# Optimization experiments

Hardware: AMD Instinct MI355X
Metric: run time of the kernel (lower is better)

Reference implementation:

```python
import jax, jax.numpy as jnp
import numpy as np

B, IN_DIM, C, H, W = 4, 64, 128, 64, 64
HW = H * W
EPS = 1e-5


def _conv(x, w, b, pad):
    y = jax.lax.conv_general_dilated(
        x, w, (1, 1), [(pad, pad), (pad, pad)],
        dimension_numbers=('NCHW', 'OIHW', 'NCHW'))
    return y + b[None, :, None, None]


def _ln_chw(x, g, b):
    # torch LayerNorm([C,H,W]): normalize over (C,H,W) per sample, affine per-element
    m = jnp.mean(x, axis=(1, 2, 3), keepdims=True)
    v = jnp.mean((x - m) ** 2, axis=(1, 2, 3), keepdims=True)
    return (x - m) * jax.lax.rsqrt(v + EPS) * g[None] + b[None]


def _lrelu(x):
    return jnp.where(x >= 0, x, 0.01 * x)


def setup_inputs():
    ks = jax.random.split(jax.random.key(0), 16)

    def n(i, shape, s):
        return jax.random.normal(ks[i], shape, jnp.float32) * s

    inp = {
        'f_e': n(0, (B, IN_DIM, H, W), 1.0),
        'f_i': n(1, (B, IN_DIM, H, W), 1.0),
        'w1': n(2, (C, IN_DIM, 3, 3), 0.04), 'b1': jnp.zeros((C,), jnp.float32),
        'g1': jnp.ones((C, H, W), jnp.float32), 'be1': jnp.zeros((C, H, W), jnp.float32),
        'w2': n(3, (C, IN_DIM, 3, 3), 0.04), 'b2': jnp.zeros((C,), jnp.float32),
        'g2': jnp.ones((C, H, W), jnp.float32), 'be2': jnp.zeros((C, H, W), jnp.float32),
        'W3': n(4, (HW, HW), 0.015), 'b3': jnp.zeros((HW,), jnp.float32),
        'W4': n(5, (C, C), 0.08), 'b4': jnp.zeros((C,), jnp.float32),
        'W5': n(6, (C, C), 0.08), 'b5': jnp.zeros((C,), jnp.float32),
        'w6a': n(7, (C, C, 1, 1), 0.08), 'b6a': jnp.zeros((C,), jnp.float32),
        'g6a': jnp.ones((C, H, W), jnp.float32), 'be6a': jnp.zeros((C, H, W), jnp.float32),
        'w6b': n(8, (C, C, 3, 3), 0.03), 'b6b': jnp.zeros((C,), jnp.float32),
        'g6b': jnp.ones((C, H, W), jnp.float32), 'be6b': jnp.zeros((C, H, W), jnp.float32),
        'wf': n(9, (IN_DIM, C, 1, 1), 0.08), 'bf': jnp.zeros((IN_DIM,), jnp.float32),
    }
    return inp


def reference(f_e, f_i, w1, b1, g1, be1, w2, b2, g2, be2, W3, b3, W4, b4,
              W5, b5, w6a, b6a, g6a, be6a, w6b, b6b, g6b, be6b, wf, bf):
    b_, _, h, w = f_e.shape
    c = w1.shape[0]
    hw = h * w

    # f_1: conv3x3 -> LN([C,H,W]) -> LeakyReLU -> b (hw) c
    x1 = _lrelu(_ln_chw(_conv(f_e, w1, b1, 1), g1, be1))
    f_e_1 = x1.transpose(0, 2, 3, 1).reshape(b_, hw, c)

    # f_2: conv3x3 -> LN -> LeakyReLU (stays b c h w)
    f_i_2 = _lrelu(_ln_chw(_conv(f_i, w2, b2, 1), g2, be2))

    # f_3: b c (hw) -> Linear(HW,HW) -> LeakyReLU
    f_i_3 = _lrelu(jnp.einsum('bcn,mn->bcm', f_i_2.reshape(b_, c, hw), W3) + b3)

    # f_4: b (hw) c -> Linear(C,C) -> LeakyReLU
    tok = f_i_2.transpose(0, 2, 3, 1).reshape(b_, hw, c)
    f_e_4 = _lrelu(jnp.einsum('bnc,dc->bnd', tok, W4) + b4)

    # unscaled single-head attention over hw tokens
    scores = jnp.einsum('bnc,bcm->bnm', f_e_4, f_i_3)   # (b, hw, hw)
    attn = jax.nn.softmax(scores, axis=-1)
    f_e_5_in = jnp.einsum('bnm,bmc->bnc', attn, f_e_1)

    # f_5: Linear(C,C) -> LeakyReLU -> b c h w
    f_e_5 = _lrelu(jnp.einsum('bnc,dc->bnd', f_e_5_in, W5) + b5)
    f_e_5 = f_e_5.reshape(b_, h, w, c).transpose(0, 3, 1, 2)

    # f_6: conv1x1 -> LN -> LReLU -> conv3x3 -> LN -> LReLU
    y = _lrelu(_ln_chw(_conv(f_i_2, w6a, b6a, 0), g6a, be6a))
    f_i_6 = _lrelu(_ln_chw(_conv(y, w6b, b6b, 1), g6b, be6b))

    f_e_7 = f_e_5 * f_i_6
    f_e_8 = _conv(f_e_7, wf, bf, 0)
    return (f_e_8, f_i_2)
```

## Files before the change

kernel.cpp:

```cpp
#include <hip/hip_runtime.h>

typedef unsigned short ushort_t;
typedef unsigned int uint_t;
typedef unsigned long long u64_t;

#define Bn 4
#define IND 64
#define Cn 128
#define Nn 4096
#define CN 524288
#define BUF 2097152

typedef __attribute__((ext_vector_type(8))) __bf16 bf16x8;
typedef __attribute__((ext_vector_type(4))) float f32x4;

__device__ __forceinline__ float b2f(ushort_t s) {
    return __uint_as_float(((uint_t)s) << 16);
}
__device__ __forceinline__ ushort_t f2b(float f) {
    uint_t u = __float_as_uint(f);
    uint_t r = u + 0x7fffu + ((u >> 16) & 1u);
    return (ushort_t)(r >> 16);
}
__device__ __forceinline__ void unpack8(uint4 u, float* f) {
    f[0] = __uint_as_float(u.x << 16); f[1] = __uint_as_float(u.x & 0xffff0000u);
    f[2] = __uint_as_float(u.y << 16); f[3] = __uint_as_float(u.y & 0xffff0000u);
    f[4] = __uint_as_float(u.z << 16); f[5] = __uint_as_float(u.z & 0xffff0000u);
    f[6] = __uint_as_float(u.w << 16); f[7] = __uint_as_float(u.w & 0xffff0000u);
}
__device__ __forceinline__ float lrelu(float x) { return x >= 0.f ? x : 0.01f * x; }

__device__ __forceinline__ float getv(const float* p, size_t i) { return p[i]; }
__device__ __forceinline__ float getv(const ushort_t* p, size_t i) { return b2f(p[i]); }
__device__ __forceinline__ float4 get4(const float* p, size_t i) { return *(const float4*)(p + i); }
__device__ __forceinline__ float4 get4(const ushort_t* p, size_t i) {
    ushort4 u = *(const ushort4*)(p + i);
    float4 f = {b2f(u.x), b2f(u.y), b2f(u.z), b2f(u.w)};
    return f;
}
__device__ __forceinline__ void stv(float* p, float v) { *p = v; }
__device__ __forceinline__ void stv(ushort_t* p, float v) { *p = f2b(v); }

__device__ __forceinline__ uint4 pack8(float4 a, float4 b) {
    uint4 r;
    r.x = (uint_t)f2b(a.x) | ((uint_t)f2b(a.y) << 16);
    r.y = (uint_t)f2b(a.z) | ((uint_t)f2b(a.w) << 16);
    r.z = (uint_t)f2b(b.x) | ((uint_t)f2b(b.y) << 16);
    r.w = (uint_t)f2b(b.z) | ((uint_t)f2b(b.w) << 16);
    return r;
}

__global__ void detect_kernel(const void* g1, int* flag) {
    if (threadIdx.x == 0 && blockIdx.x == 0)
        *flag = (((const ushort_t*)g1)[0] == 0x3F80) ? 0 : 1;
}

template <int CI>
__global__ __launch_bounds__(256) void wtrans(const void* w, ushort_t* Wt, const int* flagp) {
    int F = *flagp;
    int idx = blockIdx.x * 256 + threadIdx.x;
    if (idx >= 128 * 9 * CI) return;
    int co = idx / (9 * CI);
    int rem = idx - co * 9 * CI;
    int tap = rem / CI;
    int ci = rem - tap * CI;
    size_t srci = (size_t)co * CI * 9 + (size_t)ci * 9 + tap;
    float v = F ? ((const float*)w)[srci] : b2f(((const ushort_t*)w)[srci]);
    Wt[idx] = f2b(v);
}

template <typename TEXT>
__device__ __forceinline__ void tin_body(const TEXT* src, ushort_t* dst, float (*tile)[33]) {
    int b = blockIdx.z, c0 = blockIdx.y * 32, n0 = blockIdx.x * 32;
    int nx = threadIdx.x & 31, cy = threadIdx.x >> 5;
    #pragma unroll
    for (int s = 0; s < 4; s++) {
        int cl = cy + s * 8;
        tile[cl][nx] = getv(src, ((size_t)(b * 64 + c0 + cl)) * 4096 + n0 + nx);
    }
    __syncthreads();
    #pragma unroll
    for (int s = 0; s < 4; s++) {
        int nl = cy + s * 8;
        dst[((size_t)b * 4096 + n0 + nl) * 64 + c0 + nx] = f2b(tile[nx][nl]);
    }
}

__global__ __launch_bounds__(256) void transpose_in(const void* src, ushort_t* dst, const int* flagp) {
    __shared__ float tile[32][33];
    int F = *flagp;
    if (F) tin_body((const float*)src, dst, tile);
    else   tin_body((const ushort_t*)src, dst, tile);
}

template <int CI>
__global__ __launch_bounds__(512) void conv_mfma(const ushort_t* __restrict__ Xt,
                                                 const ushort_t* __restrict__ Wt,
                                                 const void* bias, float* __restrict__ out,
                                                 const int* flagp) {
    constexpr int RS = CI + 8;
    constexpr int SROWS = 195;
    constexpr int SBYTES = SROWS * RS * 2;
    constexpr int OBYTES = 128 * 68 * 4;
    constexpr int SMEM = SBYTES > OBYTES ? SBYTES : OBYTES;
    __shared__ __align__(16) char smem[SMEM];
    ushort_t* S = (ushort_t*)smem;
    float* Ob = (float*)smem;

    int t = threadIdx.x;
    int blk = blockIdx.x;
    int b = blk >> 6, y = blk & 63;
    int n0 = y << 6;

    constexpr int RQ = CI / 8;
    constexpr int CNT = SROWS * RQ;
    for (int i = t; i < CNT; i += 512) {
        int s = i / RQ;
        int c8 = (i - s * RQ) * 8;
        int tok = n0 + s - 65;
        uint4 v = {0u, 0u, 0u, 0u};
        if (s < 194 && (unsigned)tok < 4096u)
            v = *(const uint4*)(Xt + ((size_t)b * 4096 + tok) * CI + c8);
        *(uint4*)(S + (size_t)s * RS + c8) = v;
    }
    __syncthreads();

    int lane = t & 63, w = t >> 6;
    int li = lane & 15, q = lane >> 4;
    int px0 = 16 * (w & 3);
    int coh = 64 * (w >> 2);
    int x = px0 + li;

    f32x4 acc[4];
    #pragma unroll
    for (int T = 0; T < 4; T++) acc[T] = {0.f, 0.f, 0.f, 0.f};

    #pragma unroll
    for (int tap = 0; tap < 9; tap++) {
        int dy = tap / 3 - 1, dx = tap % 3 - 1;
        bool vx = (unsigned)(x + dx) < 64u;
        int srow = x + dy * 64 + dx + 65;
        int sr2 = vx ? srow : 194;
        #pragma unroll
        for (int ks = 0; ks < CI / 32; ks++) {
            bf16x8 a = *(const bf16x8*)(S + (size_t)sr2 * RS + ks * 32 + q * 8);
            #pragma unroll
            for (int T = 0; T < 4; T++) {
                int co = coh + 16 * T + li;
                bf16x8 bb = *(const bf16x8*)(Wt + ((size_t)co * 9 + tap) * CI + ks * 32 + q * 8);
                acc[T] = __builtin_amdgcn_mfma_f32_16x16x32_bf16(a, bb, acc[T], 0, 0, 0);
            }
        }
    }
    __syncthreads();

    int F = *flagp;
    #pragma unroll
    for (int T = 0; T < 4; T++) {
        int co = coh + 16 * T + li;
        float bv = F ? ((const float*)bias)[co] : b2f(((const ushort_t*)bias)[co]);
        #pragma unroll
        for (int rr = 0; rr < 4; rr++)
            Ob[(size_t)co * 68 + px0 + 4 * q + rr] = acc[T][rr] + bv;
    }
    __syncthreads();
    for (int i = t; i < 2048; i += 512) {
        int co = i >> 4, p4 = (i & 15) * 4;
        *(uint4*)(out + ((size_t)(b * 128 + co)) * 4096 + n0 + p4) =
            *(const uint4*)(Ob + (size_t)co * 68 + p4);
    }
}

__global__ __launch_bounds__(256) void ln_reduce1(const float* __restrict__ src,
                                                  float* __restrict__ part) {
    int t = threadIdx.x;
    size_t base = (size_t)blockIdx.x * 1024 + t * 4;
    float4 v = *(const float4*)(src + base);
    float s = v.x + v.y + v.z + v.w;
    float q = v.x * v.x + v.y * v.y + v.z * v.z + v.w * v.w;
    for (int off = 32; off > 0; off >>= 1) {
        s += __shfl_down(s, off, 64);
        q += __shfl_down(q, off, 64);
    }
    __shared__ float red[8];
    if ((t & 63) == 0) { red[(t >> 6) * 2] = s; red[(t >> 6) * 2 + 1] = q; }
    __syncthreads();
    if (t == 0) {
        s = red[0] + red[2] + red[4] + red[6];
        q = red[1] + red[3] + red[5] + red[7];
        part[blockIdx.x * 2] = s;
        part[blockIdx.x * 2 + 1] = q;
    }
}

__global__ __launch_bounds__(256) void ln_reduce2(const float* __restrict__ part,
                                                  float* __restrict__ der) {
    int b = blockIdx.x, t = threadIdx.x;
    float s = part[(b * 512 + t) * 2] + part[(b * 512 + 256 + t) * 2];
    float q = part[(b * 512 + t) * 2 + 1] + part[(b * 512 + 256 + t) * 2 + 1];
    for (int off = 32; off > 0; off >>= 1) {
        s += __shfl_down(s, off, 64);
        q += __shfl_down(q, off, 64);
    }
    __shared__ float red[8];
    if ((t & 63) == 0) { red[(t >> 6) * 2] = s; red[(t >> 6) * 2 + 1] = q; }
    __syncthreads();
    if (t == 0) {
        s = red[0] + red[2] + red[4] + red[6];
        q = red[1] + red[3] + red[5] + red[7];
        float mean = s * (1.f / (float)CN);
        float var = q * (1.f / (float)CN) - mean * mean;
        der[b * 2] = mean;
        der[b * 2 + 1] = rsqrtf(var + 1e-5f);
    }
}

template <typename TEXT, typename TOD, int HT, int HD>
__device__ __forceinline__ void ln_body(const float* src, const TEXT* g, const TEXT* be,
                                        const float* der, ushort_t* outT, TOD* outD,
                                        float (*tile)[33]) {
    int b = blockIdx.z, c0 = blockIdx.y * 32, n0 = blockIdx.x * 32;
    float mean = der[b * 2], rstd = der[b * 2 + 1];
    int nx = threadIdx.x & 31, cy = threadIdx.x >> 5;
    #pragma unroll
    for (int s = 0; s < 4; s++) {
        int cl = cy + s * 8;
        int c = c0 + cl;
        size_t gi = (size_t)c * Nn + n0 + nx;
        float v = (src[(size_t)b * CN + gi] - mean) * rstd * getv(g, gi) + getv(be, gi);
        v = lrelu(v);
        if (HD) stv(outD + (size_t)b * CN + gi, v);
        tile[cl][nx] = v;
    }
    if (HT) {
        __syncthreads();
        #pragma unroll
        for (int s = 0; s < 4; s++) {
            int nl = cy + s * 8;
            int n = n0 + nl;
            int c = c0 + nx;
            outT[((size_t)b * Nn + n) * Cn + c] = f2b(tile[nx][nl]);
        }
    }
}

template <int HT, int HD, int DEXT>
__global__ __launch_bounds__(256) void ln_apply(const float* src, const void* g, const void* be,
                                                const float* der, ushort_t* outT, void* outD,
                                                long doff, const int* flagp) {
    __shared__ float tile[32][33];
    int F = *flagp;
    if (F) {
        if (DEXT && HD)
            ln_body<float, float, HT, HD>(src, (const float*)g, (const float*)be, der, outT,
                                          ((float*)outD) + doff, tile);
        else
            ln_body<float, ushort_t, HT, HD>(src, (const float*)g, (const float*)be, der, outT,
                                             ((ushort_t*)outD) + doff, tile);
    } else {
        ln_body<ushort_t, ushort_t, HT, HD>(src, (const ushort_t*)g, (const ushort_t*)be, der, outT,
                                            ((ushort_t*)outD) + doff, tile);
    }
}

template <int ACT, int TRANS, typename TA, typename TW, typename TO>
__device__ __forceinline__ void gemm_body(const TA* A, const TW* W, const TW* bias, TO* out,
                                          int M, int K, int Rper,
                                          float (*As)[68], float (*Bs)[68]) {
    int m0 = blockIdx.x << 6, r0 = blockIdx.y << 6;
    int t = threadIdx.x, tx = t & 15, ty = t >> 4;
    int sr = t >> 2, sk = (t & 3) << 2;
    float acc[4][4] = {{0.f}};
    for (int kt = 0; kt < K; kt += 16) {
        float4 av = get4(A, (size_t)(r0 + sr) * K + kt + sk);
        float4 wv = get4(W, (size_t)(m0 + sr) * K + kt + sk);
        As[sk + 0][sr] = av.x; As[sk + 1][sr] = av.y;
        As[sk + 2][sr] = av.z; As[sk + 3][sr] = av.w;
        Bs[sk + 0][sr] = wv.x; Bs[sk + 1][sr] = wv.y;
        Bs[sk + 2][sr] = wv.z; Bs[sk + 3][sr] = wv.w;
        __syncthreads();
        #pragma unroll
        for (int kk = 0; kk < 16; kk++) {
            float4 a4 = *(const float4*)&As[kk][ty << 2];
            float4 b4 = *(const float4*)&Bs[kk][tx << 2];
            float aa[4] = {a4.x, a4.y, a4.z, a4.w};
            float bb[4] = {b4.x, b4.y, b4.z, b4.w};
            #pragma unroll
            for (int ii = 0; ii < 4; ii++)
                #pragma unroll
                for (int jj = 0; jj < 4; jj++)
                    acc[ii][jj] += aa[ii] * bb[jj];
        }
        __syncthreads();
    }
    float bv[4];
    #pragma unroll
    for (int jj = 0; jj < 4; jj++) bv[jj] = getv(bias, m0 + (tx << 2) + jj);
    #pragma unroll
    for (int ii = 0; ii < 4; ii++) {
        int r = r0 + (ty << 2) + ii;
        float v[4];
        #pragma unroll
        for (int jj = 0; jj < 4; jj++) {
            float x = acc[ii][jj] + bv[jj];
            if (ACT) x = lrelu(x);
            v[jj] = x;
        }
        if (TRANS) {
            int rb = r / Rper, ri = r % Rper;
            #pragma unroll
            for (int jj = 0; jj < 4; jj++) {
                int m = m0 + (tx << 2) + jj;
                stv(out + ((size_t)rb * M + m) * Rper + ri, v[jj]);
            }
        } else {
            #pragma unroll
            for (int jj = 0; jj < 4; jj++)
                stv(out + (size_t)r * M + m0 + (tx << 2) + jj, v[jj]);
        }
    }
}

template <int ACT, int TRANS, int AK, typename TO>
__global__ __launch_bounds__(256) void gemm_nt(const void* A, long aoff, const void* W,
                                               const void* bias, TO* out, int M, int K, int Rper,
                                               const int* flagp) {
    __shared__ float As[16][68];
    __shared__ float Bs[16][68];
    int F = *flagp;
    if (AK == 0) {
        if (F) gemm_body<ACT, TRANS>((const ushort_t*)A + aoff, (const float*)W, (const float*)bias, out, M, K, Rper, As, Bs);
        else   gemm_body<ACT, TRANS>((const ushort_t*)A + aoff, (const ushort_t*)W, (const ushort_t*)bias, out, M, K, Rper, As, Bs);
    } else if (AK == 1) {
        if (F) gemm_body<ACT, TRANS>((const float*)A + aoff, (const float*)W, (const float*)bias, out, M, K, Rper, As, Bs);
        else   gemm_body<ACT, TRANS>((const float*)A + aoff, (const ushort_t*)W, (const ushort_t*)bias, out, M, K, Rper, As, Bs);
    } else {
        if (F) gemm_body<ACT, TRANS>((const float*)A + aoff, (const float*)W, (const float*)bias, out, M, K, Rper, As, Bs);
        else   gemm_body<ACT, TRANS>((const ushort_t*)A + aoff, (const ushort_t*)W, (const ushort_t*)bias, out, M, K, Rper, As, Bs);
    }
}

template <typename TA, typename TW>
__device__ __forceinline__ void gemm_big_body(const TA* A, const TW* W3, const TW* b3,
                                              ushort_t* out, char* smem) {
    ushort_t* As = (ushort_t*)smem;
    ushort_t* Bs = (ushort_t*)(smem + 9216);
    int t = threadIdx.x;
    int m0 = blockIdx.x << 7;
    int r0 = blockIdx.y << 6;
    int lane = t & 63, w = t >> 6;
    int li = lane & 15, q = lane >> 4;
    int rs = 16 * (w & 3);
    int mh = 64 * (w >> 2);
    f32x4 acc[4];
    #pragma unroll
    for (int T = 0; T < 4; T++) acc[T] = {0.f, 0.f, 0.f, 0.f};

    int ar = t >> 3, ak8 = (t & 7) * 8;
    int br = t >> 2, bk16 = (t & 3) * 16;

    {
        size_t abase = (size_t)(r0 + ar) * 4096 + ak8;
        *(uint4*)(As + (size_t)ar * 72 + ak8) = pack8(get4(A, abase), get4(A, abase + 4));
        size_t bbase = (size_t)(m0 + br) * 4096 + bk16;
        *(uint4*)(Bs + (size_t)br * 72 + bk16) = pack8(get4(W3, bbase), get4(W3, bbase + 4));
        *(uint4*)(Bs + (size_t)br * 72 + bk16 + 8) = pack8(get4(W3, bbase + 8), get4(W3, bbase + 12));
    }
    __syncthreads();

    for (int kt = 0; kt < 4096; kt += 64) {
        float4 pa0, pa1, pb0, pb1, pb2, pb3;
        bool pf = kt < 4032;
        if (pf) {
            size_t abase = (size_t)(r0 + ar) * 4096 + kt + 64 + ak8;
            pa0 = get4(A, abase); pa1 = get4(A, abase + 4);
            size_t bbase = (size_t)(m0 + br) * 4096 + kt + 64 + bk16;
            pb0 = get4(W3, bbase); pb1 = get4(W3, bbase + 4);
            pb2 = get4(W3, bbase + 8); pb3 = get4(W3, bbase + 12);
        }
        #pragma unroll
        for (int ks = 0; ks < 2; ks++) {
            bf16x8 a = *(const bf16x8*)(As + (size_t)(rs + li) * 72 + ks * 32 + q * 8);
            #pragma unroll
            for (int T = 0; T < 4; T++) {
                bf16x8 bb = *(const bf16x8*)(Bs + (size_t)(mh + 16 * T + li) * 72 + ks * 32 + q * 8);
                acc[T] = __builtin_amdgcn_mfma_f32_16x16x32_bf16(a, bb, acc[T], 0, 0, 0);
            }
        }
        __syncthreads();
        if (pf) {
            *(uint4*)(As + (size_t)ar * 72 + ak8) = pack8(pa0, pa1);
            *(uint4*)(Bs + (size_t)br * 72 + bk16) = pack8(pb0, pb1);
            *(uint4*)(Bs + (size_t)br * 72 + bk16 + 8) = pack8(pb2, pb3);
        }
        __syncthreads();
    }

    ushort_t* Ob = (ushort_t*)smem;
    #pragma unroll
    for (int T = 0; T < 4; T++) {
        int m_l = mh + 16 * T + li;
        float bv = getv(b3, m0 + m_l);
        #pragma unroll
        for (int rr = 0; rr < 4; rr++) {
            float v = lrelu(acc[T][rr] + bv);
            Ob[(size_t)m_l * 72 + rs + 4 * q + rr] = f2b(v);
        }
    }
    __syncthreads();
    int b = r0 >> 7;
    int c0 = ((r0 >> 6) & 1) * 64;
    for (int i = t; i < 1024; i += 512) {
        int m_l = i >> 3, c8 = (i & 7) * 8;
        *(uint4*)(out + ((size_t)b * 4096 + m0 + m_l) * 128 + c0 + c8) =
            *(const uint4*)(Ob + (size_t)m_l * 72 + c8);
    }
}

__global__ __launch_bounds__(512) void gemm_big(const void* A, long aoff, const void* W3,
                                                const void* b3, ushort_t* out, const int* flagp) {
    __shared__ __align__(16) char smem[27648];
    int F = *flagp;
    if (F) gemm_big_body((const float*)A + aoff, (const float*)W3, (const float*)b3, out, smem);
    else   gemm_big_body((const ushort_t*)A + aoff, (const ushort_t*)W3, (const ushort_t*)b3, out, smem);
}

__global__ __launch_bounds__(256) void attn_mfma(const ushort_t* __restrict__ Q,
                                                 const ushort_t* __restrict__ Kg,
                                                 const ushort_t* __restrict__ Vg,
                                                 ushort_t* __restrict__ Op0,
                                                 ushort_t* __restrict__ Op1,
                                                 float* __restrict__ ML) {
    __shared__ __align__(16) ushort_t Qs[64 * 136];
    __shared__ __align__(16) ushort_t Ks[64 * 136];
    __shared__ __align__(16) ushort_t Ps[64 * 88];
    __shared__ __align__(16) ushort_t Vt[128 * 72];

    int t = threadIdx.x;
    int blk = blockIdx.x;
    int h = blk >> 8;
    int rblk = blk & 255;
    int b = (rblk >> 1) & 3;
    int qt = ((rblk >> 3) << 1) | (rblk & 1);
    int n0 = qt << 6;
    int lane = t & 63, w = t >> 6;
    int li = lane & 15, q = lane >> 4;

    int kj = t >> 2, kc0 = (t & 3) * 32;
    int vd = t >> 1, vk0 = (t & 1) * 32;

    int kt0 = h << 5;
    int m00 = kt0 << 6;

    {
        const ushort_t* qp = Q + ((size_t)(b * Nn + n0 + kj)) * 128 + kc0;
        ushort_t* dst = Qs + kj * 136 + kc0;
        #pragma unroll
        for (int cc = 0; cc < 4; cc++)
            *(uint4*)(dst + cc * 8) = *(const uint4*)(qp + cc * 8);
    }
    {
        const ushort_t* kp = Kg + ((size_t)(b * Nn + m00 + kj)) * 128 + kc0;
        ushort_t* dst = Ks + kj * 136 + kc0;
        #pragma unroll
        for (int cc = 0; cc < 4; cc++)
            *(uint4*)(dst + cc * 8) = *(const uint4*)(kp + cc * 8);
    }
    {
        const ushort_t* vp = Vg + (size_t)b * CN + (size_t)vd * Nn + m00 + vk0;
        ushort_t* dst = Vt + vd * 72 + vk0;
        #pragma unroll
        for (int cc = 0; cc < 4; cc++)
            *(uint4*)(dst + cc * 8) = *(const uint4*)(vp + cc * 8);
    }

    f32x4 acc[8];
    #pragma unroll
    for (int T = 0; T < 8; T++) acc[T] = {0.f, 0.f, 0.f, 0.f};
    float m_i[4], l_i[4];
    #pragma unroll
    for (int r = 0; r < 4; r++) { m_i[r] = -1e30f; l_i[r] = 0.f; }

    __syncthreads();

    bf16x8 qf[4];
    #pragma unroll
    for (int ks = 0; ks < 4; ks++)
        qf[ks] = *(const bf16x8*)(Qs + (16 * w + li) * 136 + ks * 32 + q * 8);

    for (int kt = kt0; kt < kt0 + 32; kt++) {
        uint4 pk[4], pv[4];
        bool pf = kt < kt0 + 31;
        if (pf) {
            int m1 = (kt + 1) << 6;
            const ushort_t* kp = Kg + ((size_t)(b * Nn + m1 + kj)) * 128 + kc0;
            #pragma unroll
            for (int cc = 0; cc < 4; cc++) pk[cc] = *(const uint4*)(kp + cc * 8);
            const ushort_t* vp = Vg + (size_t)b * CN + (size_t)vd * Nn + m1 + vk0;
            #pragma unroll
            for (int cc = 0; cc < 4; cc++) pv[cc] = *(const uint4*)(vp + cc * 8);
        }

        f32x4 s[4];
        #pragma unroll
        for (int T = 0; T < 4; T++) s[T] = {0.f, 0.f, 0.f, 0.f};
        __builtin_amdgcn_s_setprio(1);
        #pragma unroll
        for (int ks = 0; ks < 4; ks++) {
            bf16x8 a = qf[ks];
            #pragma unroll
            for (int T = 0; T < 4; T++) {
                bf16x8 bb = *(const bf16x8*)(Ks + (16 * T + li) * 136 + ks * 32 + q * 8);
                s[T] = __builtin_amdgcn_mfma_f32_16x16x32_bf16(a, bb, s[T], 0, 0, 0);
            }
        }
        __builtin_amdgcn_s_setprio(0);

        float p[4][4];
        float rm4[4];
        #pragma unroll
        for (int r = 0; r < 4; r++) {
            float rm = fmaxf(fmaxf(s[0][r], s[1][r]), fmaxf(s[2][r], s[3][r]));
            rm = fmaxf(rm, __shfl_xor(rm, 1, 64));
            rm = fmaxf(rm, __shfl_xor(rm, 2, 64));
            rm = fmaxf(rm, __shfl_xor(rm, 4, 64));
            rm = fmaxf(rm, __shfl_xor(rm, 8, 64));
            rm4[r] = rm;
        }
        bool grow = (rm4[0] > m_i[0]) | (rm4[1] > m_i[1]) |
                    (rm4[2] > m_i[2]) | (rm4[3] > m_i[3]);
        if (__any(grow)) {
            float al[4];
            #pragma unroll
            for (int r = 0; r < 4; r++) {
                float mnew = fmaxf(m_i[r], rm4[r]);
                al[r] = __expf(m_i[r] - mnew);
                m_i[r] = mnew;
                float rsum = 0.f;
                #pragma unroll
                for (int T = 0; T < 4; T++) {
                    float pvv = __expf(s[T][r] - mnew);
                    p[T][r] = pvv;
                    rsum += pvv;
                }
                l_i[r] = l_i[r] * al[r] + rsum;
            }
            #pragma unroll
            for (int T = 0; T < 8; T++)
                #pragma unroll
                for (int r = 0; r < 4; r++)
                    acc[T][r] *= al[r];
        } else {
            #pragma unroll
            for (int r = 0; r < 4; r++) {
                float rsum = 0.f;
                #pragma unroll
                for (int T = 0; T < 4; T++) {
                    float pvv = __expf(s[T][r] - m_i[r]);
                    p[T][r] = pvv;
                    rsum += pvv;
                }
                l_i[r] += rsum;
            }
        }
        #pragma unroll
        for (int T = 0; T < 4; T++)
            #pragma unroll
            for (int r = 0; r < 4; r++)
                Ps[(16 * w + 4 * q + r) * 88 + 16 * T + li] = f2b(p[T][r]);

        __builtin_amdgcn_s_setprio(1);
        #pragma unroll
        for (int ks = 0; ks < 2; ks++) {
            bf16x8 a = *(const bf16x8*)(Ps + (16 * w + li) * 88 + ks * 32 + q * 8);
            #pragma unroll
            for (int T = 0; T < 8; T++) {
                bf16x8 bv = *(const bf16x8*)(Vt + (16 * T + li) * 72 + ks * 32 + q * 8);
                acc[T] = __builtin_amdgcn_mfma_f32_16x16x32_bf16(a, bv, acc[T], 0, 0, 0);
            }
        }
        __builtin_amdgcn_s_setprio(0);
        __syncthreads();
        if (pf) {
            ushort_t* dk = Ks + kj * 136 + kc0;
            #pragma unroll
            for (int cc = 0; cc < 4; cc++) *(uint4*)(dk + cc * 8) = pk[cc];
            ushort_t* dv = Vt + vd * 72 + vk0;
            #pragma unroll
            for (int cc = 0; cc < 4; cc++) *(uint4*)(dv + cc * 8) = pv[cc];
            __syncthreads();
        }
    }

    #pragma unroll
    for (int r = 0; r < 4; r++) {
        float ls = l_i[r];
        ls += __shfl_xor(ls, 1, 64);
        ls += __shfl_xor(ls, 2, 64);
        ls += __shfl_xor(ls, 4, 64);
        ls += __shfl_xor(ls, 8, 64);
        l_i[r] = ls;
    }

    ushort_t* Op = h ? Op1 : Op0;
    #pragma unroll
    for (int T = 0; T < 8; T++)
        #pragma unroll
        for (int r = 0; r < 4; r++) {
            int n = n0 + 16 * w + 4 * q + r;
            int d = 16 * T + li;
            Op[((size_t)(b * Nn + n)) * 128 + d] = f2b(acc[T][r]);
        }
    if (li == 0) {
        #pragma unroll
        for (int r = 0; r < 4; r++) {
            int n = n0 + 16 * w + 4 * q + r;
            size_t mi = ((size_t)(h * Bn + b) * Nn + n) * 2;
            ML[mi] = m_i[r];
            ML[mi + 1] = l_i[r];
        }
    }
}

__global__ __launch_bounds__(256) void attn_merge(const ushort_t* __restrict__ Op0,
                                                  const ushort_t* __restrict__ Op1,
                                                  const float* __restrict__ ML,
                                                  float* __restrict__ Og) {
    int idx = blockIdx.x * 256 + threadIdx.x;
    int token = idx >> 4;
    int c8 = (idx & 15) * 8;
    float m0 = ML[(size_t)token * 2], l0 = ML[(size_t)token * 2 + 1];
    float m1 = ML[((size_t)Bn * Nn + token) * 2];
    float l1 = ML[((size_t)Bn * Nn + token) * 2 + 1];
    float M = fmaxf(m0, m1);
    float e0 = __expf(m0 - M), e1 = __expf(m1 - M);
    float denom = l0 * e0 + l1 * e1;
    float s0 = e0 / denom, s1 = e1 / denom;
    uint4 u0 = *(const uint4*)(Op0 + (size_t)token * 128 + c8);
    uint4 u1 = *(const uint4*)(Op1 + (size_t)token * 128 + c8);
    float f0[8], f1[8];
    unpack8(u0, f0);
    unpack8(u1, f1);
    float o[8];
    #pragma unroll
    for (int j = 0; j < 8; j++) o[j] = f0[j] * s0 + f1[j] * s1;
    float4 v0 = {o[0], o[1], o[2], o[3]};
    float4 v1 = {o[4], o[5], o[6], o[7]};
    float* op = Og + (size_t)token * 128 + c8;
    *(float4*)op = v0;
    *(float4*)(op + 4) = v1;
}

template <typename TEXT, typename TOUT>
__device__ __forceinline__ void final_body(const ushort_t* fe5, const ushort_t* fi6t,
                                           const TEXT* wf, const TEXT* bf, TOUT* out0,
                                           float* prod, ushort_t* wfs, float* bfs) {
    int t = threadIdx.x;
    int b = blockIdx.x >> 6;
    int px0 = (blockIdx.x & 63) * 64;
    for (int idx = t * 4; idx < 8192; idx += 1024) {
        float4 v = get4(wf, idx);
        ushort4 u = {f2b(v.x), f2b(v.y), f2b(v.z), f2b(v.w)};
        *(ushort4*)&wfs[idx] = u;
    }
    if (t < 64) bfs[t] = getv(bf, t);
    {
        int pix = t >> 2, kc = (t & 3) * 32;
        const ushort_t* ap = fe5 + ((size_t)(b * Nn + px0 + pix)) * 128 + kc;
        const ushort_t* bp = fi6t + ((size_t)(b * Nn + px0 + pix)) * 128 + kc;
        #pragma unroll
        for (int c = 0; c < 4; c++) {
            uint4 ua = *(const uint4*)(ap + c * 8);
            uint4 ub = *(const uint4*)(bp + c * 8);
            float fa[8], fb[8];
            unpack8(ua, fa);
            unpack8(ub, fb);
            float* pp = &prod[pix * 132 + kc + c * 8];
            #pragma unroll
            for (int j = 0; j < 8; j++) pp[j] = fa[j] * fb[j];
        }
    }
    __syncthreads();
    int pix = t >> 2, og = t & 3;
    for (int k = 0; k < 16; k++) {
        int o = og * 16 + k;
        float a = bfs[o];
        for (int kc = 0; kc < 128; kc += 8) {
            uint4 wu = *(const uint4*)&wfs[o * 128 + kc];
            float w8[8];
            unpack8(wu, w8);
            const float* pp = &prod[pix * 132 + kc];
            float4 p0 = *(const float4*)pp;
            float4 p1 = *(const float4*)(pp + 4);
            a += w8[0] * p0.x + w8[1] * p0.y + w8[2] * p0.z + w8[3] * p0.w
               + w8[4] * p1.x + w8[5] * p1.y + w8[6] * p1.z + w8[7] * p1.w;
        }
        stv(out0 + ((size_t)(b * 64 + o)) * Nn + px0 + pix, a);
    }
}

__global__ __launch_bounds__(256) void final_out(const ushort_t* fe5, const ushort_t* fi6t,
                                                 const void* wf, const void* bf, void* out0,
                                                 const int* flagp) {
    __shared__ __align__(16) float prod[64 * 132];
    __shared__ __align__(16) ushort_t wfs[64 * 128];
    __shared__ float bfs[64];
    int F = *flagp;
    if (F) final_body((const ushort_t*)fe5, fi6t, (const float*)wf, (const float*)bf, (float*)out0, prod, wfs, bfs);
    else   final_body((const ushort_t*)fe5, fi6t, (const ushort_t*)wf, (const ushort_t*)bf, (ushort_t*)out0, prod, wfs, bfs);
}

extern "C" void kernel_launch(void* const* d_in, const int* in_sizes, int n_in,
                              void* d_out, int out_size, void* d_ws, size_t ws_size,
                              hipStream_t stream) {
    const void* f_e = d_in[0];
    const void* f_i = d_in[1];
    const void* w1 = d_in[2];
    const void* b1 = d_in[3];
    const void* g1 = d_in[4];
    const void* be1 = d_in[5];
    const void* w2 = d_in[6];
    const void* b2 = d_in[7];
    const void* g2 = d_in[8];
    const void* be2 = d_in[9];
    const void* W3 = d_in[10];
    const void* b3 = d_in[11];
    const void* W4 = d_in[12];
    const void* b4 = d_in[13];
    const void* W5 = d_in[14];
    const void* b5 = d_in[15];
    const void* w6a = d_in[16];
    const void* b6a = d_in[17];
    const void* g6a = d_in[18];
    const void* be6a = d_in[19];
    const void* w6b = d_in[20];
    const void* b6b = d_in[21];
    const void* g6b = d_in[22];
    const void* be6b = d_in[23];
    const void* wf = d_in[24];
    const void* bf = d_in[25];

    char* wsb = (char*)d_ws;
    int* FLAG = (int*)wsb;
    float* PART = (float*)(wsb + 1024);
    float* DER  = (float*)(wsb + 17408);
    ushort_t* Wt1  = (ushort_t*)(wsb + 32768);
    ushort_t* Wt2  = (ushort_t*)(wsb + 180224);
    ushort_t* Wt6b = (ushort_t*)(wsb + 327680);
    float* ML   = (float*)(wsb + 32768);
    float* TMP  = (float*)(wsb + 622592);
    ushort_t* FE1  = (ushort_t*)(wsb + 9011200);
    ushort_t* TOK  = FE1 + BUF;
    ushort_t* FI3T = TOK + BUF;
    ushort_t* FE4  = FI3T + BUF;
    ushort_t* Y6   = FE4 + BUF;
    ushort_t* FI6T = Y6 + BUF;

    ushort_t* FEt = FI3T;
    ushort_t* FIt = FE4;

    const long OUT1OFF = (long)Bn * IND * Nn;

    dim3 lnGrid(128, 4, 4);
    dim3 tinGrid(128, 2, 4);

    detect_kernel<<<1, 64, 0, stream>>>(g1, FLAG);

    wtrans<64><<<288, 256, 0, stream>>>(w1, Wt1, FLAG);
    wtrans<64><<<288, 256, 0, stream>>>(w2, Wt2, FLAG);
    wtrans<128><<<576, 256, 0, stream>>>(w6b, Wt6b, FLAG);

    transpose_in<<<tinGrid, 256, 0, stream>>>(f_e, FEt, FLAG);
    conv_mfma<64><<<256, 512, 0, stream>>>(FEt, Wt1, b1, TMP, FLAG);
    ln_reduce1<<<2048, 256, 0, stream>>>(TMP, PART);
    ln_reduce2<<<4, 256, 0, stream>>>(PART, DER);
    ln_apply<0, 1, 0><<<lnGrid, 256, 0, stream>>>(TMP, g1, be1, DER, nullptr, FE1, 0, FLAG);

    transpose_in<<<tinGrid, 256, 0, stream>>>(f_i, FIt, FLAG);
    conv_mfma<64><<<256, 512, 0, stream>>>(FIt, Wt2, b2, TMP, FLAG);
    ln_reduce1<<<2048, 256, 0, stream>>>(TMP, PART);
    ln_reduce2<<<4, 256, 0, stream>>>(PART, DER);
    ln_apply<1, 1, 1><<<lnGrid, 256, 0, stream>>>(TMP, g2, be2, DER, TOK, d_out, OUT1OFF, FLAG);

    gemm_big<<<dim3(32, 8), 512, 0, stream>>>(d_out, OUT1OFF, W3, b3, FI3T, FLAG);

    gemm_nt<1, 0, 0, ushort_t><<<dim3(2, 256), 256, 0, stream>>>(TOK, 0, W4, b4, FE4, 128, 128, 1, FLAG);

    gemm_nt<0, 1, 0, float><<<dim3(2, 256), 256, 0, stream>>>(TOK, 0, w6a, b6a, TMP, 128, 128, 4096, FLAG);
    ln_reduce1<<<2048, 256, 0, stream>>>(TMP, PART);
    ln_reduce2<<<4, 256, 0, stream>>>(PART, DER);
    ln_apply<1, 0, 0><<<lnGrid, 256, 0, stream>>>(TMP, g6a, be6a, DER, Y6, nullptr, 0, FLAG);

    conv_mfma<128><<<256, 512, 0, stream>>>(Y6, Wt6b, b6b, TMP, FLAG);
    ln_reduce1<<<2048, 256, 0, stream>>>(TMP, PART);
    ln_reduce2<<<4, 256, 0, stream>>>(PART, DER);
    ln_apply<1, 0, 0><<<lnGrid, 256, 0, stream>>>(TMP, g6b, be6b, DER, FI6T, nullptr, 0, FLAG);

    attn_mfma<<<512, 256, 0, stream>>>(FE4, FI3T, FE1, TOK, Y6, ML);
    attn_merge<<<1024, 256, 0, stream>>>(TOK, Y6, ML, TMP);

    gemm_nt<1, 0, 1, ushort_t><<<dim3(2, 256), 256, 0, stream>>>(TMP, 0, W5, b5, Y6, 128, 128, 1, FLAG);

    final_out<<<256, 256, 0, stream>>>(Y6, FI6T, wf, bf, d_out, FLAG);
}
```

Before: 590.1 us.

## Enlarge attention query tile to 128 rows and split keys four ways

The flash-attention kernel now gives each block 128 query rows (two 16-row sub-tiles per wave) instead of 64, so every K/V tile loaded to shared memory is reused across twice as many queries. The key dimension is split into four chunks of 16 tiles instead of two of 32, which keeps the grid at 512 blocks. The merge kernel now combines four partial outputs. Q fragments are read straight from global memory, and the extra partial buffers reuse the TMP and FI3T regions. The cost is more accumulator registers per thread and more merge traffic.

```diff
diff --git a/kernel.cpp b/kernel.cpp
--- a/kernel.cpp
+++ b/kernel.cpp
@@ -425,40 +425,34 @@
     else   gemm_big_body((const ushort_t*)A + aoff, (const ushort_t*)W3, (const ushort_t*)b3, out, smem);
 }
 
-__global__ __launch_bounds__(256) void attn_mfma(const ushort_t* __restrict__ Q,
-                                                 const ushort_t* __restrict__ Kg,
-                                                 const ushort_t* __restrict__ Vg,
-                                                 ushort_t* __restrict__ Op0,
-                                                 ushort_t* __restrict__ Op1,
-                                                 float* __restrict__ ML) {
-    __shared__ __align__(16) ushort_t Qs[64 * 136];
+__global__ __launch_bounds__(256, 2) void attn_mfma(const ushort_t* __restrict__ Q,
+                                                    const ushort_t* __restrict__ Kg,
+                                                    const ushort_t* __restrict__ Vg,
+                                                    ushort_t* __restrict__ Op0,
+                                                    ushort_t* __restrict__ Op1,
+                                                    ushort_t* __restrict__ Op2,
+                                                    ushort_t* __restrict__ Op3,
+                                                    float* __restrict__ ML) {
     __shared__ __align__(16) ushort_t Ks[64 * 136];
-    __shared__ __align__(16) ushort_t Ps[64 * 88];
     __shared__ __align__(16) ushort_t Vt[128 * 72];
+    __shared__ __align__(16) ushort_t Ps[128 * 88];
 
     int t = threadIdx.x;
     int blk = blockIdx.x;
-    int h = blk >> 8;
-    int rblk = blk & 255;
-    int b = (rblk >> 1) & 3;
-    int qt = ((rblk >> 3) << 1) | (rblk & 1);
-    int n0 = qt << 6;
+    int h = blk >> 7;
+    int rblk = blk & 127;
+    int b = rblk & 3;
+    int qt = rblk >> 2;
+    int n0 = qt << 7;
     int lane = t & 63, w = t >> 6;
     int li = lane & 15, q = lane >> 4;
 
     int kj = t >> 2, kc0 = (t & 3) * 32;
     int vd = t >> 1, vk0 = (t & 1) * 32;
 
-    int kt0 = h << 5;
+    int kt0 = h << 4;
     int m00 = kt0 << 6;
 
-    {
-        const ushort_t* qp = Q + ((size_t)(b * Nn + n0 + kj)) * 128 + kc0;
-        ushort_t* dst = Qs + kj * 136 + kc0;
-        #pragma unroll
-        for (int cc = 0; cc < 4; cc++)
-            *(uint4*)(dst + cc * 8) = *(const uint4*)(qp + cc * 8);
-    }
     {
         const ushort_t* kp = Kg + ((size_t)(b * Nn + m00 + kj)) * 128 + kc0;
         ushort_t* dst = Ks + kj * 136 + kc0;
@@ -474,23 +468,30 @@
             *(uint4*)(dst + cc * 8) = *(const uint4*)(vp + cc * 8);
     }
 
-    f32x4 acc[8];
-    #pragma unroll
-    for (int T = 0; T < 8; T++) acc[T] = {0.f, 0.f, 0.f, 0.f};
-    float m_i[4], l_i[4];
-    #pragma unroll
-    for (int r = 0; r < 4; r++) { m_i[r] = -1e30f; l_i[r] = 0.f; }
-
-    __syncthreads();
-
-    bf16x8 qf[4];
-    #pragma unroll
-    for (int ks = 0; ks < 4; ks++)
-        qf[ks] = *(const bf16x8*)(Qs + (16 * w + li) * 136 + ks * 32 + q * 8);
-
-    for (int kt = kt0; kt < kt0 + 32; kt++) {
+    bf16x8 qf[2][4];
+    #pragma unroll
+    for (int sub = 0; sub < 2; sub++)
+        #pragma unroll
+        for (int ks = 0; ks < 4; ks++)
+            qf[sub][ks] = *(const bf16x8*)(Q +
+                ((size_t)(b * Nn + n0 + 32 * w + 16 * sub + li)) * 128 + ks * 32 + q * 8);
+
+    f32x4 acc[2][8];
+    #pragma unroll
+    for (int sub = 0; sub < 2; sub++)
+        #pragma unroll
+        for (int T = 0; T < 8; T++) acc[sub][T] = {0.f, 0.f, 0.f, 0.f};
+    float m_i[2][4], l_i[2][4];
+    #pragma unroll
+    for (int sub = 0; sub < 2; sub++)
+        #pragma unroll
+        for (int r = 0; r < 4; r++) { m_i[sub][r] = -1e30f; l_i[sub][r] = 0.f; }
+
+    __syncthreads();
+
+    for (int kt = kt0; kt < kt0 + 16; kt++) {
         uint4 pk[4], pv[4];
-        bool pf = kt < kt0 + 31;
+        bool pf = kt < kt0 + 15;
         if (pf) {
             int m1 = (kt + 1) << 6;
             const ushort_t* kp = Kg + ((size_t)(b * Nn + m1 + kj)) * 128 + kc0;
@@ -501,82 +502,85 @@
             for (int cc = 0; cc < 4; cc++) pv[cc] = *(const uint4*)(vp + cc * 8);
         }
 
-        f32x4 s[4];
-        #pragma unroll
-        for (int T = 0; T < 4; T++) s[T] = {0.f, 0.f, 0.f, 0.f};
+        f32x4 s[2][4];
+        #pragma unroll
+        for (int sub = 0; sub < 2; sub++)
+            #pragma unroll
+            for (int T = 0; T < 4; T++) s[sub][T] = {0.f, 0.f, 0.f, 0.f};
         __builtin_amdgcn_s_setprio(1);
         #pragma unroll
         for (int ks = 0; ks < 4; ks++) {
-            bf16x8 a = qf[ks];
+            bf16x8 a0 = qf[0][ks];
+            bf16x8 a1 = qf[1][ks];
             #pragma unroll
             for (int T = 0; T < 4; T++) {
-                bf16x8 bb = *(const bf16x8*)(Ks + (16 * T + li) * 136 + ks * 32 + q * 8);
-                s[T] = __builtin_amdgcn_mfma_f32_16x16x32_bf16(a, bb, s[T], 0, 0, 0);
+                bf16x8 kb = *(const bf16x8*)(Ks + (16 * T + li) * 136 + ks * 32 + q * 8);
+                s[0][T] = __builtin_amdgcn_mfma_f32_16x16x32_bf16(a0, kb, s[0][T], 0, 0, 0);
+                s[1][T] = __builtin_amdgcn_mfma_f32_16x16x32_bf16(a1, kb, s[1][T], 0, 0, 0);
             }
         }
         __builtin_amdgcn_s_setprio(0);
 
-        float p[4][4];
-        float rm4[4];
-        #pragma unroll
-        for (int r = 0; r < 4; r++) {
-            float rm = fmaxf(fmaxf(s[0][r], s[1][r]), fmaxf(s[2][r], s[3][r]));
-            rm = fmaxf(rm, __shfl_xor(rm, 1, 64));
-            rm = fmaxf(rm, __shfl_xor(rm, 2, 64));
-            rm = fmaxf(rm, __shfl_xor(rm, 4, 64));
-            rm = fmaxf(rm, __shfl_xor(rm, 8, 64));
-            rm4[r] = rm;
-        }
-        bool grow = (rm4[0] > m_i[0]) | (rm4[1] > m_i[1]) |
-                    (rm4[2] > m_i[2]) | (rm4[3] > m_i[3]);
+        float rm[2][4];
+        bool grow = false;
+        #pragma unroll
+        for (int sub = 0; sub < 2; sub++)
+            #pragma unroll
+            for (int r = 0; r < 4; r++) {
+                float v = fmaxf(fmaxf(s[sub][0][r], s[sub][1][r]),
+                                fmaxf(s[sub][2][r], s[sub][3][r]));
+                v = fmaxf(v, __shfl_xor(v, 1, 64));
+                v = fmaxf(v, __shfl_xor(v, 2, 64));
+                v = fmaxf(v, __shfl_xor(v, 4, 64));
+                v = fmaxf(v, __shfl_xor(v, 8, 64));
+                rm[sub][r] = v;
+                grow = grow || (v > m_i[sub][r]);
+            }
         if (__any(grow)) {
-            float al[4];
-            #pragma unroll
-            for (int r = 0; r < 4; r++) {
-                float mnew = fmaxf(m_i[r], rm4[r]);
-                al[r] = __expf(m_i[r] - mnew);
-                m_i[r] = mnew;
-                float rsum = 0.f;
+            #pragma unroll
+            for (int sub = 0; sub < 2; sub++)
                 #pragma unroll
-                for (int T = 0; T < 4; T++) {
-                    float pvv = __expf(s[T][r] - mnew);
-                    p[T][r] = pvv;
-                    rsum += pvv;
+                for (int r = 0; r < 4; r++) {
+                    float mnew = fmaxf(m_i[sub][r], rm[sub][r]);
+                    float al = __expf(m_i[sub][r] - mnew);
+                    m_i[sub][r] = mnew;
+                    float rsum = 0.f;
+                    #pragma unroll
+                    for (int T = 0; T < 4; T++) {
+                        float pvv = __expf(s[sub][T][r] - mnew);
+                        Ps[(32 * w + 16 * sub + 4 * q + r) * 88 + 16 * T + li] = f2b(pvv);
+                        rsum += pvv;
+                    }
+                    l_i[sub][r] = l_i[sub][r] * al + rsum;
+                    #pragma unroll
+                    for (int T = 0; T < 8; T++) acc[sub][T][r] *= al;
                 }
-                l_i[r] = l_i[r] * al[r] + rsum;
-            }
-            #pragma unroll
-            for (int T = 0; T < 8; T++)
+        } else {
+            #pragma unroll
+            for (int sub = 0; sub < 2; sub++)
                 #pragma unroll
-                for (int r = 0; r < 4; r++)
-                    acc[T][r] *= al[r];
-        } else {
-            #pragma unroll
-            for (int r = 0; r < 4; r++) {
-                float rsum = 0.f;
-                #pragma unroll
-                for (int T = 0; T < 4; T++) {
-                    float pvv = __expf(s[T][r] - m_i[r]);
-                    p[T][r] = pvv;
-                    rsum += pvv;
+                for (int r = 0; r < 4; r++) {
+                    float rsum = 0.f;
+                    #pragma unroll
+                    for (int T = 0; T < 4; T++) {
+                        float pvv = __expf(s[sub][T][r] - m_i[sub][r]);
+                        Ps[(32 * w + 16 * sub + 4 * q + r) * 88 + 16 * T + li] = f2b(pvv);
+                        rsum += pvv;
+                    }
+                    l_i[sub][r] += rsum;
                 }
-                l_i[r] += rsum;
-            }
-        }
-        #pragma unroll
-        for (int T = 0; T < 4; T++)
-            #pragma unroll
-            for (int r = 0; r < 4; r++)
-                Ps[(16 * w + 4 * q + r) * 88 + 16 * T + li] = f2b(p[T][r]);
+        }
 
         __builtin_amdgcn_s_setprio(1);
         #pragma unroll
         for (int ks = 0; ks < 2; ks++) {
-            bf16x8 a = *(const bf16x8*)(Ps + (16 * w + li) * 88 + ks * 32 + q * 8);
+            bf16x8 pa0 = *(const bf16x8*)(Ps + (32 * w + li) * 88 + ks * 32 + q * 8);
+            bf16x8 pa1 = *(const bf16x8*)(Ps + (32 * w + 16 + li) * 88 + ks * 32 + q * 8);
             #pragma unroll
             for (int T = 0; T < 8; T++) {
-                bf16x8 bv = *(const bf16x8*)(Vt + (16 * T + li) * 72 + ks * 32 + q * 8);
-                acc[T] = __builtin_amdgcn_mfma_f32_16x16x32_bf16(a, bv, acc[T], 0, 0, 0);
+                bf16x8 vb = *(const bf16x8*)(Vt + (16 * T + li) * 72 + ks * 32 + q * 8);
+                acc[0][T] = __builtin_amdgcn_mfma_f32_16x16x32_bf16(pa0, vb, acc[0][T], 0, 0, 0);
+                acc[1][T] = __builtin_amdgcn_mfma_f32_16x16x32_bf16(pa1, vb, acc[1][T], 0, 0, 0);
             }
         }
         __builtin_amdgcn_s_setprio(0);
@@ -593,57 +597,77 @@
     }
 
     #pragma unroll
-    for (int r = 0; r < 4; r++) {
-        float ls = l_i[r];
-        ls += __shfl_xor(ls, 1, 64);
-        ls += __shfl_xor(ls, 2, 64);
-        ls += __shfl_xor(ls, 4, 64);
-        ls += __shfl_xor(ls, 8, 64);
-        l_i[r] = ls;
-    }
-
-    ushort_t* Op = h ? Op1 : Op0;
-    #pragma unroll
-    for (int T = 0; T < 8; T++)
+    for (int sub = 0; sub < 2; sub++)
         #pragma unroll
         for (int r = 0; r < 4; r++) {
-            int n = n0 + 16 * w + 4 * q + r;
-            int d = 16 * T + li;
-            Op[((size_t)(b * Nn + n)) * 128 + d] = f2b(acc[T][r]);
-        }
+            float ls = l_i[sub][r];
+            ls += __shfl_xor(ls, 1, 64);
+            ls += __shfl_xor(ls, 2, 64);
+            ls += __shfl_xor(ls, 4, 64);
+            ls += __shfl_xor(ls, 8, 64);
+            l_i[sub][r] = ls;
+        }
+
+    ushort_t* Op = (h == 0) ? Op0 : (h == 1) ? Op1 : (h == 2) ? Op2 : Op3;
+    #pragma unroll
+    for (int sub = 0; sub < 2; sub++)
+        #pragma unroll
+        for (int T = 0; T < 8; T++)
+            #pragma unroll
+            for (int r = 0; r < 4; r++) {
+                int n = n0 + 32 * w + 16 * sub + 4 * q + r;
+                int d = 16 * T + li;
+                Op[((size_t)(b * Nn + n)) * 128 + d] = f2b(acc[sub][T][r]);
+            }
     if (li == 0) {
         #pragma unroll
-        for (int r = 0; r < 4; r++) {
-            int n = n0 + 16 * w + 4 * q + r;
-            size_t mi = ((size_t)(h * Bn + b) * Nn + n) * 2;
-            ML[mi] = m_i[r];
-            ML[mi + 1] = l_i[r];
-        }
+        for (int sub = 0; sub < 2; sub++)
+            #pragma unroll
+            for (int r = 0; r < 4; r++) {
+                int n = n0 + 32 * w + 16 * sub + 4 * q + r;
+                size_t mi = ((size_t)(h * Bn + b) * Nn + n) * 2;
+                ML[mi] = m_i[sub][r];
+                ML[mi + 1] = l_i[sub][r];
+            }
     }
 }
 
 __global__ __launch_bounds__(256) void attn_merge(const ushort_t* __restrict__ Op0,
                                                   const ushort_t* __restrict__ Op1,
+                                                  const ushort_t* __restrict__ Op2,
+                                                  const ushort_t* __restrict__ Op3,
                                                   const float* __restrict__ ML,
                                                   float* __restrict__ Og) {
     int idx = blockIdx.x * 256 + threadIdx.x;
     int token = idx >> 4;
     int c8 = (idx & 15) * 8;
-    float m0 = ML[(size_t)token * 2], l0 = ML[(size_t)token * 2 + 1];
-    float m1 = ML[((size_t)Bn * Nn + token) * 2];
-    float l1 = ML[((size_t)Bn * Nn + token) * 2 + 1];
-    float M = fmaxf(m0, m1);
-    float e0 = __expf(m0 - M), e1 = __expf(m1 - M);
-    float denom = l0 * e0 + l1 * e1;
-    float s0 = e0 / denom, s1 = e1 / denom;
+    float m[4], l[4];
+    #pragma unroll
+    for (int s = 0; s < 4; s++) {
+        m[s] = ML[((size_t)s * (Bn * Nn) + token) * 2];
+        l[s] = ML[((size_t)s * (Bn * Nn) + token) * 2 + 1];
+    }
+    float M = fmaxf(fmaxf(m[0], m[1]), fmaxf(m[2], m[3]));
+    float e[4];
+    float denom = 0.f;
+    #pragma unroll
+    for (int s = 0; s < 4; s++) { e[s] = __expf(m[s] - M); denom += l[s] * e[s]; }
+    float inv = 1.f / denom;
+    #pragma unroll
+    for (int s = 0; s < 4; s++) e[s] *= inv;
     uint4 u0 = *(const uint4*)(Op0 + (size_t)token * 128 + c8);
     uint4 u1 = *(const uint4*)(Op1 + (size_t)token * 128 + c8);
-    float f0[8], f1[8];
+    uint4 u2 = *(const uint4*)(Op2 + (size_t)token * 128 + c8);
+    uint4 u3 = *(const uint4*)(Op3 + (size_t)token * 128 + c8);
+    float f0[8], f1[8], f2[8], f3[8];
     unpack8(u0, f0);
     unpack8(u1, f1);
+    unpack8(u2, f2);
+    unpack8(u3, f3);
     float o[8];
     #pragma unroll
-    for (int j = 0; j < 8; j++) o[j] = f0[j] * s0 + f1[j] * s1;
+    for (int j = 0; j < 8; j++)
+        o[j] = f0[j] * e[0] + f1[j] * e[1] + f2[j] * e[2] + f3[j] * e[3];
     float4 v0 = {o[0], o[1], o[2], o[3]};
     float4 v1 = {o[4], o[5], o[6], o[7]};
     float* op = Og + (size_t)token * 128 + c8;
@@ -759,6 +783,10 @@
     ushort_t* FEt = FI3T;
     ushort_t* FIt = FE4;
 
+    ushort_t* OPA = (ushort_t*)TMP;
+    ushort_t* OPB = OPA + BUF;
+    float* MRG = (float*)FI3T;
+
     const long OUT1OFF = (long)Bn * IND * Nn;
 
     dim3 lnGrid(128, 4, 4);
@@ -796,10 +824,10 @@
     ln_reduce2<<<4, 256, 0, stream>>>(PART, DER);
     ln_apply<1, 0, 0><<<lnGrid, 256, 0, stream>>>(TMP, g6b, be6b, DER, FI6T, nullptr, 0, FLAG);
 
-    attn_mfma<<<512, 256, 0, stream>>>(FE4, FI3T, FE1, TOK, Y6, ML);
-    attn_merge<<<1024, 256, 0, stream>>>(TOK, Y6, ML, TMP);
-
-    gemm_nt<1, 0, 1, ushort_t><<<dim3(2, 256), 256, 0, stream>>>(TMP, 0, W5, b5, Y6, 128, 128, 1, FLAG);
+    attn_mfma<<<512, 256, 0, stream>>>(FE4, FI3T, FE1, TOK, Y6, OPA, OPB, ML);
+    attn_merge<<<1024, 256, 0, stream>>>(TOK, Y6, OPA, OPB, ML, MRG);
+
+    gemm_nt<1, 0, 1, ushort_t><<<dim3(2, 256), 256, 0, stream>>>(MRG, 0, W5, b5, Y6, 128, 128, 1, FLAG);
 
     final_out<<<256, 256, 0, stream>>>(Y6, FI6T, wf, bf, d_out, FLAG);
 }
```

Measured after the change: 569.5 us. 3.5% less time.
